# Performance work log

Measured on AMD Instinct MI355X. Metric: run time of the kernel, lower is better.

## Reference

```python
import jax, jax.numpy as jnp
import numpy as np
import math

D_MODEL = 1024
NHEAD = 16
FACTOR = 5


def setup_inputs() -> dict:
    key = jax.random.key(0)
    kq, kk, kv = jax.random.split(key, 3)
    B, L = 4, 2048
    Q = jax.random.normal(kq, (B, L, D_MODEL), dtype=jnp.float32)
    K = jax.random.normal(kk, (B, L, D_MODEL), dtype=jnp.float32)
    V = jax.random.normal(kv, (B, L, D_MODEL), dtype=jnp.float32)
    return {"Q": Q, "K": K, "V": V}


def reference(Q, K, V):
    B, q_len, _ = Q.shape
    k_len = K.shape[1]
    head_dim = D_MODEL // NHEAD
    scale = 1.0 / math.sqrt(head_dim)

    # [B, H, L, Dh]
    Qh = Q.reshape(B, q_len, NHEAD, head_dim).transpose(0, 2, 1, 3)
    Kh = K.reshape(B, k_len, NHEAD, head_dim).transpose(0, 2, 1, 3)
    Vh = V.reshape(B, k_len, NHEAD, head_dim).transpose(0, 2, 1, 3)

    # Dense scores for KL-based query selection
    scores = jnp.einsum('bhqd,bhkd->bhqk', Qh, Kh) * scale
    logp = jax.nn.log_softmax(scores, axis=-1)
    probs = jnp.exp(logp)
    # KL(p || uniform) = sum p * (log p + log k_len)
    kl_div = jnp.sum(probs * (logp + jnp.log(jnp.float32(k_len))), axis=-1)  # [B,H,Q]

    top_u = min(int(FACTOR * math.log(q_len)), q_len)
    _, indices = jax.lax.top_k(kl_div, top_u)  # [B,H,U]

    # Gather selected queries
    Q_sparse = jnp.take_along_axis(Qh, indices[..., None], axis=2)  # [B,H,U,Dh]
    scores_sparse = jnp.einsum('bhud,bhkd->bhuk', Q_sparse, Kh) * scale
    attn_weights = jax.nn.softmax(scores_sparse, axis=-1)  # dropout p=0 (eval)
    output_sparse = jnp.einsum('bhuk,bhkd->bhud', attn_weights, Vh)

    # Scatter back into full-length output (non-selected queries are zero)
    b_idx = jnp.arange(B)[:, None, None]
    h_idx = jnp.arange(NHEAD)[None, :, None]
    output_full = jnp.zeros_like(Qh).at[b_idx, h_idx, indices].set(output_sparse)

    output = output_full.transpose(0, 2, 1, 3).reshape(B, q_len, D_MODEL)
    return output, attn_weights
```

## Files before the change

### kernel.cpp

```cpp
#include <hip/hip_runtime.h>
#include <math.h>

#define LQ 2048
#define DM 1024
#define NH 16
#define DH 64
#define UU 38
#define NBH 64
#define SCALE 0.125f

typedef _Float16 f16x8 __attribute__((ext_vector_type(8)));
typedef float f32x4 __attribute__((ext_vector_type(4)));

#if __has_builtin(__builtin_amdgcn_exp2f)
#define EXP2F(x) __builtin_amdgcn_exp2f(x)
#else
#define EXP2F(x) exp2f(x)
#endif

#define F_OFF_SEL   4194304
#define F_OFF_L3    4204032
#define F_OFF_MASK  4213760
#define F_OFF_LPART 4344832
#define F_OFF_KSP   7146496
#define F_NEED      40700928ull

__global__ __launch_bounds__(256) void ksplit_kernel(const float* __restrict__ K,
                                                     _Float16* __restrict__ ksp) {
  int idx = blockIdx.x * 256 + threadIdx.x;
  int p = idx & 7;
  int k = (idx >> 3) & 63;
  int kc = (idx >> 9) & 31;
  int bh = idx >> 14;
  int b = bh >> 4, h = bh & 15;
  const float* src = K + ((size_t)(b * LQ + kc * 64 + k)) * DM + h * DH + (p ^ (k & 7)) * 8;
  float4 x0 = *(const float4*)src;
  float4 x1 = *(const float4*)(src + 4);
  f16x8 hi, lo;
#define KCV(i, xx) { float x_ = (xx); _Float16 hh = (_Float16)x_; hi[i] = hh; lo[i] = (_Float16)(x_ - (float)hh); }
  KCV(0, x0.x) KCV(1, x0.y) KCV(2, x0.z) KCV(3, x0.w)
  KCV(4, x1.x) KCV(5, x1.y) KCV(6, x1.z) KCV(7, x1.w)
#undef KCV
  _Float16* base = ksp + ((size_t)(bh * 32 + kc)) * 8192;
  *(f16x8*)(base + k * 64 + p * 8) = hi;
  *(f16x8*)(base + 4096 + k * 64 + p * 8) = lo;
}

__global__ __launch_bounds__(256) void kl_mfma2(const float* __restrict__ Q,
                                                const _Float16* __restrict__ ksp,
                                                double* __restrict__ lt) {
  int bh = blockIdx.x & 63;
  int qc = (blockIdx.x >> 6) & 15;
  int sp = blockIdx.x >> 10;
  int b = bh >> 4, h = bh & 15;
  int t = threadIdx.x;
  int lane = t & 63, w = t >> 6;
  int quad = lane >> 4, l15 = lane & 15;

  __shared__ __align__(16) _Float16 kbuf[8192];

  f16x8 ahi[2][2], alo[2][2];
  {
    const float* qrow = Q + ((size_t)(b * LQ + qc * 128)) * DM + h * DH;
#pragma unroll
    for (int qt = 0; qt < 2; ++qt)
#pragma unroll
      for (int c = 0; c < 2; ++c) {
        const float* p = qrow + (size_t)(w * 32 + qt * 16 + l15) * DM + c * 32 + quad * 8;
        float4 x0 = *(const float4*)p;
        float4 x1 = *(const float4*)(p + 4);
        f16x8 hi, lo;
#define QCV(i, xx) { float x_ = (xx); _Float16 hh = (_Float16)x_; hi[i] = hh; lo[i] = (_Float16)(x_ - (float)hh); }
        QCV(0, x0.x) QCV(1, x0.y) QCV(2, x0.z) QCV(3, x0.w)
        QCV(4, x1.x) QCV(5, x1.y) QCV(6, x1.z) QCV(7, x1.w)
#undef QCV
        ahi[qt][c] = hi;
        alo[qt][c] = lo;
      }
  }

  int bsw0 = quad ^ (l15 & 7);
  int bsw1 = (quad + 4) ^ (l15 & 7);
  _Float16* khi = kbuf;
  _Float16* klo = kbuf + 4096;
  const float C1 = 0.18033688011112042f;

  double l64[2][4], t64[2][4];
#pragma unroll
  for (int qt = 0; qt < 2; ++qt)
#pragma unroll
    for (int r = 0; r < 4; ++r) { l64[qt][r] = 0.0; t64[qt][r] = 0.0; }

  const uint4* gbase = (const uint4*)(ksp + ((size_t)(bh * 32 + sp * 16)) * 8192);
  uint4* lbuf = (uint4*)kbuf;

  for (int c = 0; c < 16; ++c) {
    const uint4* gsrc = gbase + (size_t)c * 1024;
    __syncthreads();
#pragma unroll
    for (int i = 0; i < 4; ++i) lbuf[i * 256 + t] = gsrc[i * 256 + t];
    __syncthreads();

    float l32[2][4], t32[2][4];
#pragma unroll
    for (int qt = 0; qt < 2; ++qt)
#pragma unroll
      for (int r = 0; r < 4; ++r) { l32[qt][r] = 0.f; t32[qt][r] = 0.f; }

#pragma unroll
    for (int kt = 0; kt < 4; ++kt) {
      int key = kt * 16 + l15;
      f16x8 bhi0 = *(const f16x8*)(khi + key * 64 + bsw0 * 8);
      f16x8 bhi1 = *(const f16x8*)(khi + key * 64 + bsw1 * 8);
      f16x8 blo0 = *(const f16x8*)(klo + key * 64 + bsw0 * 8);
      f16x8 blo1 = *(const f16x8*)(klo + key * 64 + bsw1 * 8);
#pragma unroll
      for (int qt = 0; qt < 2; ++qt) {
        f32x4 cacc = {0.f, 0.f, 0.f, 0.f};
        cacc = __builtin_amdgcn_mfma_f32_16x16x32_f16(alo[qt][0], bhi0, cacc, 0, 0, 0);
        cacc = __builtin_amdgcn_mfma_f32_16x16x32_f16(alo[qt][1], bhi1, cacc, 0, 0, 0);
        cacc = __builtin_amdgcn_mfma_f32_16x16x32_f16(ahi[qt][0], blo0, cacc, 0, 0, 0);
        cacc = __builtin_amdgcn_mfma_f32_16x16x32_f16(ahi[qt][1], blo1, cacc, 0, 0, 0);
        cacc = __builtin_amdgcn_mfma_f32_16x16x32_f16(ahi[qt][0], bhi0, cacc, 0, 0, 0);
        cacc = __builtin_amdgcn_mfma_f32_16x16x32_f16(ahi[qt][1], bhi1, cacc, 0, 0, 0);
#pragma unroll
        for (int r = 0; r < 4; ++r) {
          float rr = cacc[r];
          float e = EXP2F(rr * C1);
          l32[qt][r] += e;
          t32[qt][r] = fmaf(rr, e, t32[qt][r]);
        }
      }
    }
#pragma unroll
    for (int qt = 0; qt < 2; ++qt)
#pragma unroll
      for (int r = 0; r < 4; ++r) {
        l64[qt][r] += (double)l32[qt][r];
        t64[qt][r] += (double)t32[qt][r];
      }
  }

#pragma unroll
  for (int qt = 0; qt < 2; ++qt)
#pragma unroll
    for (int r = 0; r < 4; ++r) {
      double lv = l64[qt][r], tv = t64[qt][r];
#pragma unroll
      for (int m = 1; m < 16; m <<= 1) {
        lv += __shfl_xor(lv, m);
        tv += __shfl_xor(tv, m);
      }
      if (l15 == 0) {
        int qg = qc * 128 + w * 32 + qt * 16 + quad * 4 + r;
        double* dst = lt + ((size_t)(sp * 64 + bh) * LQ + qg) * 2;
        dst[0] = lv;
        dst[1] = tv;
      }
    }
}

__global__ __launch_bounds__(64) void topk2(const double* __restrict__ lt,
                                            int* __restrict__ idxout,
                                            signed char* __restrict__ selmask) {
  int bh = blockIdx.x;
  int lane = threadIdx.x;
  __shared__ double vals[LQ];
  const double logL = 7.624618986159398;
  double bv = -INFINITY;
  int bi = LQ;
  for (int j = 0; j < 32; ++j) {
    int i = j * 64 + lane;
    const double* p0 = lt + ((size_t)bh * LQ + i) * 2;
    const double* p1 = lt + ((size_t)(64 + bh) * LQ + i) * 2;
    double l = p0[0] + p1[0];
    double tt = p0[1] + p1[1];
    double v = 0.125 * (tt / l) - log(l) + logL;
    vals[i] = v;
    selmask[bh * LQ + i] = -1;
    if (v > bv) { bv = v; bi = i; }
  }
  for (int u = 0; u < UU; ++u) {
    double gv = bv;
    int gi = bi;
#pragma unroll
    for (int m = 1; m < 64; m <<= 1) {
      double ov = __shfl_xor(gv, m);
      int oi = __shfl_xor(gi, m);
      if (ov > gv || (ov == gv && oi < gi)) { gv = ov; gi = oi; }
    }
    if (lane == 0) {
      idxout[bh * UU + u] = gi;
      selmask[bh * LQ + gi] = (signed char)u;
    }
    if ((gi & 63) == lane) {
      vals[gi] = -INFINITY;
      bv = -INFINITY;
      bi = LQ;
      for (int j = 0; j < 32; ++j) {
        int i = j * 64 + lane;
        double v = vals[i];
        if (v > bv) { bv = v; bi = i; }
      }
    }
  }
}

__global__ __launch_bounds__(256) void attn_w_mfma(const float* __restrict__ Q,
                                                   const _Float16* __restrict__ ksp,
                                                   const int* __restrict__ sel,
                                                   float* __restrict__ wout,
                                                   float* __restrict__ lpart) {
  int bh = blockIdx.x >> 4;
  int ks = blockIdx.x & 15;
  int b = bh >> 4, h = bh & 15;
  int t = threadIdx.x;
  int lane = t & 63, w = t >> 6;
  int quad = lane >> 4, l15 = lane & 15;

  __shared__ __align__(16) _Float16 kbuf[8192];
  __shared__ float els[48 * 132];
  __shared__ int sidx[UU];

  if (t < UU) sidx[t] = sel[bh * UU + t];
  __syncthreads();

  f16x8 ahi[3][2], alo[3][2];
#pragma unroll
  for (int qt = 0; qt < 3; ++qt) {
    int u = qt * 16 + l15;
    if (u > 37) u = 37;
    const float* qrow = Q + ((size_t)(b * LQ + sidx[u])) * DM + h * DH;
#pragma unroll
    for (int c = 0; c < 2; ++c) {
      const float* p = qrow + c * 32 + quad * 8;
      float4 x0 = *(const float4*)p;
      float4 x1 = *(const float4*)(p + 4);
      f16x8 hi, lo;
#define QCV(i, xx) { float x_ = (xx); _Float16 hh = (_Float16)x_; hi[i] = hh; lo[i] = (_Float16)(x_ - (float)hh); }
      QCV(0, x0.x) QCV(1, x0.y) QCV(2, x0.z) QCV(3, x0.w)
      QCV(4, x1.x) QCV(5, x1.y) QCV(6, x1.z) QCV(7, x1.w)
#undef QCV
      ahi[qt][c] = hi;
      alo[qt][c] = lo;
    }
  }

  int bsw0 = quad ^ (l15 & 7);
  int bsw1 = (quad + 4) ^ (l15 & 7);
  const float C1 = 0.18033688011112042f;
  const uint4* gbase = (const uint4*)(ksp + ((size_t)(bh * 32 + ks * 2)) * 8192);
  uint4* lbuf = (uint4*)kbuf;
  _Float16* khi = kbuf;
  _Float16* klo = kbuf + 4096;

  for (int chunk = 0; chunk < 2; ++chunk) {
    __syncthreads();
#pragma unroll
    for (int i = 0; i < 4; ++i) lbuf[i * 256 + t] = gbase[chunk * 1024 + i * 256 + t];
    __syncthreads();
    int key = w * 16 + l15;
    f16x8 bhi0 = *(const f16x8*)(khi + key * 64 + bsw0 * 8);
    f16x8 bhi1 = *(const f16x8*)(khi + key * 64 + bsw1 * 8);
    f16x8 blo0 = *(const f16x8*)(klo + key * 64 + bsw0 * 8);
    f16x8 blo1 = *(const f16x8*)(klo + key * 64 + bsw1 * 8);
#pragma unroll
    for (int qt = 0; qt < 3; ++qt) {
      f32x4 cacc = {0.f, 0.f, 0.f, 0.f};
      cacc = __builtin_amdgcn_mfma_f32_16x16x32_f16(alo[qt][0], bhi0, cacc, 0, 0, 0);
      cacc = __builtin_amdgcn_mfma_f32_16x16x32_f16(alo[qt][1], bhi1, cacc, 0, 0, 0);
      cacc = __builtin_amdgcn_mfma_f32_16x16x32_f16(ahi[qt][0], blo0, cacc, 0, 0, 0);
      cacc = __builtin_amdgcn_mfma_f32_16x16x32_f16(ahi[qt][1], blo1, cacc, 0, 0, 0);
      cacc = __builtin_amdgcn_mfma_f32_16x16x32_f16(ahi[qt][0], bhi0, cacc, 0, 0, 0);
      cacc = __builtin_amdgcn_mfma_f32_16x16x32_f16(ahi[qt][1], bhi1, cacc, 0, 0, 0);
#pragma unroll
      for (int r = 0; r < 4; ++r) {
        float e = EXP2F(cacc[r] * C1);
        els[(qt * 16 + quad * 4 + r) * 132 + chunk * 64 + w * 16 + l15] = e;
      }
    }
  }
  __syncthreads();

  for (int i = t; i < UU * 128; i += 256) {
    int u = i >> 7, k = i & 127;
    wout[((size_t)(bh * UU + u)) * LQ + ks * 128 + k] = els[u * 132 + k];
  }

#pragma unroll
  for (int p = 0; p < 10; ++p) {
    int u = w + 4 * p;
    if (u < UU) {
      float s = els[u * 132 + lane] + els[u * 132 + 64 + lane];
#pragma unroll
      for (int m = 1; m < 64; m <<= 1) s += __shfl_xor(s, m);
      if (lane == 0) lpart[(bh * 16 + ks) * UU + u] = s;
    }
  }
}

__global__ __launch_bounds__(256) void attn_pv2(const float* __restrict__ V,
                                                const float* __restrict__ wout,
                                                const float* __restrict__ lpart,
                                                float* __restrict__ opart,
                                                float* __restrict__ l3) {
  int bh = blockIdx.x >> 4;
  int ks = blockIdx.x & 15;
  int b = bh >> 4, h = bh & 15;
  int t = threadIdx.x;
  int d = t & 63, ug = t >> 6;

  if (ks == 0 && t < UU) {
    float s = 0.f;
#pragma unroll
    for (int i = 0; i < 16; ++i) s += lpart[(bh * 16 + i) * UU + t];
    l3[bh * UU + t] = s;
  }

  __shared__ float ps[40 * 132];
  for (int i = t; i < UU * 32; i += 256) {
    int u = i >> 5, d4 = i & 31;
    *(float4*)(ps + u * 132 + d4 * 4) =
        *(const float4*)(wout + ((size_t)(bh * UU + u)) * LQ + ks * 128 + d4 * 4);
  }
  for (int i = t; i < 2 * 132; i += 256) ps[UU * 132 + i] = 0.f;
  __syncthreads();

  const float* vbase = V + ((size_t)(b * LQ + ks * 128)) * DM + h * DH + d;
  float o[10];
#pragma unroll
  for (int p = 0; p < 10; ++p) o[p] = 0.f;

  for (int j4 = 0; j4 < 128; j4 += 4) {
    float v0 = vbase[(size_t)(j4 + 0) * DM];
    float v1 = vbase[(size_t)(j4 + 1) * DM];
    float v2 = vbase[(size_t)(j4 + 2) * DM];
    float v3 = vbase[(size_t)(j4 + 3) * DM];
#pragma unroll
    for (int p = 0; p < 10; ++p) {
      float4 pw = *(const float4*)(ps + (ug + 4 * p) * 132 + j4);
      o[p] = fmaf(pw.x, v0, o[p]);
      o[p] = fmaf(pw.y, v1, o[p]);
      o[p] = fmaf(pw.z, v2, o[p]);
      o[p] = fmaf(pw.w, v3, o[p]);
    }
  }

#pragma unroll
  for (int p = 0; p < 10; ++p) {
    int u = ug + 4 * p;
    if (u < UU) opart[((size_t)((bh * 16 + ks) * UU + u)) * DH + d] = o[p];
  }
}

__global__ __launch_bounds__(256) void writeout_kernel(const signed char* __restrict__ selmask,
                                                       const float* __restrict__ l3,
                                                       const float* __restrict__ opart,
                                                       float* __restrict__ out,
                                                       float* __restrict__ wout) {
  const int N1 = NBH * UU * LQ;
  int i = blockIdx.x * 256 + threadIdx.x;
  if (i < N1) {
    wout[i] = wout[i] / l3[i >> 11];
  } else {
    int i2 = i - N1;
    int d = i2 & 63;
    int h = (i2 >> 6) & 15;
    int q = (i2 >> 10) & 2047;
    int b = i2 >> 21;
    int bh = b * 16 + h;
    int u = selmask[bh * LQ + q];
    float val = 0.f;
    if (u >= 0) {
      float s = 0.f;
#pragma unroll
      for (int p = 0; p < 16; ++p)
        s += opart[((size_t)((bh * 16 + p) * UU + u)) * DH + d];
      val = s / l3[bh * UU + u];
    }
    out[i2] = val;
  }
}

extern "C" void kernel_launch(void* const* d_in, const int* in_sizes, int n_in,
                              void* d_out, int out_size, void* d_ws, size_t ws_size,
                              hipStream_t stream) {
  (void)in_sizes; (void)n_in;
  if (ws_size < F_NEED) return;
  const float* Q = (const float*)d_in[0];
  const float* K = (const float*)d_in[1];
  const float* V = (const float*)d_in[2];
  float* out = (float*)d_out;
  float* wout = out + (size_t)4 * LQ * DM;
  char* ws = (char*)d_ws;

  double* lt = (double*)ws;
  int* sel = (int*)(ws + F_OFF_SEL);
  float* l3 = (float*)(ws + F_OFF_L3);
  signed char* mask = (signed char*)(ws + F_OFF_MASK);
  float* lpart = (float*)(ws + F_OFF_LPART);
  _Float16* ksp = (_Float16*)(ws + F_OFF_KSP);
  float* opart = (float*)(ws + F_OFF_KSP);

  ksplit_kernel<<<4096, 256, 0, stream>>>(K, ksp);
  kl_mfma2<<<2048, 256, 0, stream>>>(Q, ksp, lt);
  topk2<<<NBH, 64, 0, stream>>>(lt, sel, mask);
  attn_w_mfma<<<NBH * 16, 256, 0, stream>>>(Q, ksp, sel, wout, lpart);
  attn_pv2<<<NBH * 16, 256, 0, stream>>>(V, wout, lpart, opart, l3);
  writeout_kernel<<<(NBH * UU * LQ + 4 * LQ * DM) / 256, 256, 0, stream>>>(
      mask, l3, opart, out, wout);
}
```

Baseline: 363.0 us.

## Prefetch K chunks into registers, trim els LDS, vectorize writeout with float4

The KL kernel now loads the next K chunk into registers while the current chunk is computed, so global load latency overlaps with the MFMA work. attn_w_mfma shrinks its exp buffer to 38 rows and skips the exp for padded rows. writeout_kernel is vectorized to float4 and multiplies by a reciprocal instead of dividing. These changes add register pressure in the KL kernel, and the reciprocal can change rounding slightly.

```diff
diff --git a/kernel.cpp b/kernel.cpp
--- a/kernel.cpp
+++ b/kernel.cpp
@@ -94,12 +94,20 @@
   const uint4* gbase = (const uint4*)(ksp + ((size_t)(bh * 32 + sp * 16)) * 8192);
   uint4* lbuf = (uint4*)kbuf;
 
+  uint4 pref[4];
+#pragma unroll
+  for (int i = 0; i < 4; ++i) pref[i] = gbase[i * 256 + t];
+
   for (int c = 0; c < 16; ++c) {
-    const uint4* gsrc = gbase + (size_t)c * 1024;
     __syncthreads();
 #pragma unroll
-    for (int i = 0; i < 4; ++i) lbuf[i * 256 + t] = gsrc[i * 256 + t];
+    for (int i = 0; i < 4; ++i) lbuf[i * 256 + t] = pref[i];
     __syncthreads();
+    if (c + 1 < 16) {
+      const uint4* gsrc = gbase + (size_t)(c + 1) * 1024;
+#pragma unroll
+      for (int i = 0; i < 4; ++i) pref[i] = gsrc[i * 256 + t];
+    }
 
     float l32[2][4], t32[2][4];
 #pragma unroll
@@ -219,7 +227,7 @@
   int quad = lane >> 4, l15 = lane & 15;
 
   __shared__ __align__(16) _Float16 kbuf[8192];
-  __shared__ float els[48 * 132];
+  __shared__ float els[UU * 132];
   __shared__ int sidx[UU];
 
   if (t < UU) sidx[t] = sel[bh * UU + t];
@@ -275,8 +283,11 @@
       cacc = __builtin_amdgcn_mfma_f32_16x16x32_f16(ahi[qt][1], bhi1, cacc, 0, 0, 0);
 #pragma unroll
       for (int r = 0; r < 4; ++r) {
-        float e = EXP2F(cacc[r] * C1);
-        els[(qt * 16 + quad * 4 + r) * 132 + chunk * 64 + w * 16 + l15] = e;
+        int u = qt * 16 + quad * 4 + r;
+        if (u < UU) {
+          float e = EXP2F(cacc[r] * C1);
+          els[u * 132 + chunk * 64 + w * 16 + l15] = e;
+        }
       }
     }
   }
@@ -358,27 +369,35 @@
                                                        const float* __restrict__ opart,
                                                        float* __restrict__ out,
                                                        float* __restrict__ wout) {
-  const int N1 = NBH * UU * LQ;
+  const int N1v = (NBH * UU * LQ) / 4;
   int i = blockIdx.x * 256 + threadIdx.x;
-  if (i < N1) {
-    wout[i] = wout[i] / l3[i >> 11];
+  if (i < N1v) {
+    float inv = 1.0f / l3[i >> 9];
+    float4 v = ((const float4*)wout)[i];
+    v.x *= inv; v.y *= inv; v.z *= inv; v.w *= inv;
+    ((float4*)wout)[i] = v;
   } else {
-    int i2 = i - N1;
-    int d = i2 & 63;
-    int h = (i2 >> 6) & 15;
-    int q = (i2 >> 10) & 2047;
-    int b = i2 >> 21;
-    int bh = b * 16 + h;
-    int u = selmask[bh * LQ + q];
-    float val = 0.f;
-    if (u >= 0) {
-      float s = 0.f;
-#pragma unroll
-      for (int p = 0; p < 16; ++p)
-        s += opart[((size_t)((bh * 16 + p) * UU + u)) * DH + d];
-      val = s / l3[bh * UU + u];
-    }
-    out[i2] = val;
+    int i2 = i - N1v;
+    if (i2 < (4 * LQ * DM) / 4) {
+      int h = (i2 >> 4) & 15;
+      int q = (i2 >> 8) & 2047;
+      int b = i2 >> 19;
+      int bh = b * 16 + h;
+      int u = selmask[bh * LQ + q];
+      float4 val = make_float4(0.f, 0.f, 0.f, 0.f);
+      if (u >= 0) {
+        int d4 = i2 & 15;
+        float4 s = make_float4(0.f, 0.f, 0.f, 0.f);
+#pragma unroll
+        for (int p = 0; p < 16; ++p) {
+          float4 t4 = *(const float4*)(opart + ((size_t)((bh * 16 + p) * UU + u)) * DH + d4 * 4);
+          s.x += t4.x; s.y += t4.y; s.z += t4.z; s.w += t4.w;
+        }
+        float inv = 1.0f / l3[bh * UU + u];
+        val = make_float4(s.x * inv, s.y * inv, s.z * inv, s.w * inv);
+      }
+      ((float4*)out)[i2] = val;
+    }
   }
 }
 
@@ -407,6 +426,6 @@
   topk2<<<NBH, 64, 0, stream>>>(lt, sel, mask);
   attn_w_mfma<<<NBH * 16, 256, 0, stream>>>(Q, ksp, sel, wout, lpart);
   attn_pv2<<<NBH * 16, 256, 0, stream>>>(V, wout, lpart, opart, l3);
-  writeout_kernel<<<(NBH * UU * LQ + 4 * LQ * DM) / 256, 256, 0, stream>>>(
-      mask, l3, opart, out, wout);
-}
+  int nv = (NBH * UU * LQ) / 4 + (4 * LQ * DM) / 4;
+  writeout_kernel<<<(nv + 255) / 256, 256, 0, stream>>>(mask, l3, opart, out, wout);
+}
```

Measured after the change: 401.0 us. 10.5% more time.
